# Performance work log

Measured on AMD Instinct MI355X. Metric: run time of the kernel, lower is better.

The kernel has to match this reference:

```python
import jax, jax.numpy as jnp
import numpy as np

N = 8192
IN_F = 512
OUT_F = 64
NEG_SLOPE = 0.01  # nn.LeakyReLU default
MASK_VAL = -1e9


def setup_inputs() -> dict:
    key = jax.random.key(0)
    k_h, k_adj, k_W, k_a = jax.random.split(key, 4)
    h = jax.random.normal(k_h, (N, IN_F), dtype=jnp.float32)
    adjacency = jax.random.randint(k_adj, (N, N), 0, 2, dtype=jnp.int32)
    # xavier_uniform bounds
    bW = float(np.sqrt(6.0 / (IN_F + OUT_F)))
    ba = float(np.sqrt(6.0 / (2 * OUT_F + 1)))
    W = jax.random.uniform(k_W, (IN_F, OUT_F), minval=-bW, maxval=bW, dtype=jnp.float32)
    a = jax.random.uniform(k_a, (2 * OUT_F, 1), minval=-ba, maxval=ba, dtype=jnp.float32)
    return {"h": h, "adjacency": adjacency, "W": W, "a": a}


def reference(h, adjacency, W, a):
    WH = h @ W                                  # [N, out_f]
    wh1 = WH @ a[:OUT_F, :]                     # [N, 1]
    wh2 = WH @ a[OUT_F:, :]                     # [N, 1]
    e = jax.nn.leaky_relu(wh1 + wh2.T, negative_slope=NEG_SLOPE)  # [N, N]
    attnt = jnp.where(adjacency > 0, e, jnp.float32(MASK_VAL))
    attnt = jax.nn.softmax(attnt, axis=1)       # row-wise softmax
    hfirst = attnt @ WH                         # [N, out_f]
    return jax.nn.elu(hfirst)
```

## Files before the change

### kernel.cpp

```cpp
#include <hip/hip_runtime.h>
#include <hip/hip_bf16.h>

#define N 8192
#define IN_F 512
#define OUT_F 64
#define S_SPLIT 16
#define JT (N / S_SPLIT)
#define NB (N / 8)
#define LDP 536
#define WHB 128
#define PACKB ((N / 32) * (N / 256) * 4)
#define LOG2E 1.44269504088896340736f

typedef __attribute__((ext_vector_type(8))) short short8;
typedef __attribute__((ext_vector_type(4))) float floatx4;
typedef __attribute__((ext_vector_type(4))) int intx4;

__device__ inline short f2bf(float x) {
    __hip_bfloat16 b = __float2bfloat16(x);
    return __builtin_bit_cast(short, b);
}

__device__ inline float fexp2(float x) {
#if __has_builtin(__builtin_amdgcn_exp2f)
    return __builtin_amdgcn_exp2f(x);
#else
    return exp2f(x);
#endif
}

__global__ void k_wt(const float* __restrict__ W, short* __restrict__ WT) {
    int idx = blockIdx.x * 256 + threadIdx.x;
    int k = idx >> 6, f = idx & 63;
    WT[f * IN_F + k] = f2bf(W[k * OUT_F + f]);
}

__global__ __launch_bounds__(256) void k_packwh(const int* __restrict__ adj,
                                                unsigned* __restrict__ mask,
                                                const float* __restrict__ h,
                                                const short* __restrict__ WT,
                                                const float* __restrict__ a,
                                                short* __restrict__ WHbT,
                                                float* __restrict__ wh1,
                                                float* __restrict__ wh2) {
    __shared__ float tileS[4][OUT_F][17];
    int tid = threadIdx.x;

    if (blockIdx.x >= WHB) {
        int bid = blockIdx.x - WHB;
        int wv = (bid * 256 + tid) >> 6;
        int lane = tid & 63;
        const int* p = adj + (size_t)wv * 512 + lane;
        unsigned long long m0 = __ballot(p[0]   > 0);
        unsigned long long m1 = __ballot(p[64]  > 0);
        unsigned long long m2 = __ballot(p[128] > 0);
        unsigned long long m3 = __ballot(p[192] > 0);
        unsigned long long m4 = __ballot(p[256] > 0);
        unsigned long long m5 = __ballot(p[320] > 0);
        unsigned long long m6 = __ballot(p[384] > 0);
        unsigned long long m7 = __ballot(p[448] > 0);
        if (lane < 16) {
            unsigned long long s0 = (lane & 2) ? m1 : m0;
            unsigned long long s1 = (lane & 2) ? m3 : m2;
            unsigned long long s2 = (lane & 2) ? m5 : m4;
            unsigned long long s3 = (lane & 2) ? m7 : m6;
            unsigned long long t0 = (lane & 4) ? s1 : s0;
            unsigned long long t1 = (lane & 4) ? s3 : s2;
            unsigned long long u  = (lane & 8) ? t1 : t0;
            unsigned dw = (lane & 1) ? (unsigned)(u >> 32) : (unsigned)u;
            mask[wv * 16 + lane] = dw;
        }
        return;
    }

    int w = tid >> 6, lane = tid & 63;
    int n = lane & 15, q = lane >> 4;
    int i0 = (blockIdx.x * 4 + w) * 16;
    float (*tile)[17] = tileS[w];
    const float* hp = h + (size_t)(i0 + n) * IN_F + q * 8;
    floatx4 acc[4] = {};
#pragma unroll
    for (int k0 = 0; k0 < IN_F; k0 += 32) {
        floatx4 h0 = *(const floatx4*)(hp + k0);
        floatx4 h1 = *(const floatx4*)(hp + k0 + 4);
        short8 af;
#pragma unroll
        for (int j = 0; j < 4; j++) { af[j] = f2bf(h0[j]); af[j + 4] = f2bf(h1[j]); }
#pragma unroll
        for (int b = 0; b < 4; b++) {
            short8 bf_ = *(const short8*)(WT + (b * 16 + n) * IN_F + k0 + q * 8);
            acc[b] = __builtin_amdgcn_mfma_f32_16x16x32_bf16(af, bf_, acc[b], 0, 0, 0);
        }
    }
#pragma unroll
    for (int b = 0; b < 4; b++)
#pragma unroll
        for (int r = 0; r < 4; r++)
            tile[b * 16 + n][q * 4 + r] = acc[b][r];
    float a1v[4], a2v[4];
#pragma unroll
    for (int b = 0; b < 4; b++) { a1v[b] = a[b * 16 + n]; a2v[b] = a[OUT_F + b * 16 + n]; }
#pragma unroll
    for (int r = 0; r < 4; r++) {
        float s1 = 0.f, s2 = 0.f;
#pragma unroll
        for (int b = 0; b < 4; b++) { s1 += acc[b][r] * a1v[b]; s2 += acc[b][r] * a2v[b]; }
#pragma unroll
        for (int m = 1; m <= 8; m <<= 1) {
            s1 += __shfl_xor(s1, m, 64);
            s2 += __shfl_xor(s2, m, 64);
        }
        if (n == 0) {
            wh1[i0 + q * 4 + r] = s1 * LOG2E;
            wh2[i0 + q * 4 + r] = s2 * LOG2E;
        }
    }
    __syncthreads();
    const float* tc = tile[lane & 63];
    short8 s0, s1v;
#pragma unroll
    for (int k = 0; k < 8; k++) { s0[k] = f2bf(tc[k]); s1v[k] = f2bf(tc[k + 8]); }
    *(short8*)(WHbT + (size_t)lane * N + i0) = s0;
    *(short8*)(WHbT + (size_t)lane * N + i0 + 8) = s1v;
}

__global__ __launch_bounds__(256, 2) void k_attn(const unsigned char* __restrict__ mask,
                                                 const short* __restrict__ WHbT,
                                                 const float* __restrict__ wh1,
                                                 const float* __restrict__ wh2,
                                                 float* __restrict__ num_part,
                                                 float* __restrict__ den_part) {
    __shared__ short ldsb[OUT_F * LDP];
    int tid = threadIdx.x;
    int w = tid >> 6;
    int lane = tid & 63;
    int n = lane & 15, q = lane >> 4;
    int split = blockIdx.y;
    int j0 = split * JT;
    int i0 = blockIdx.x * 256 + w * 64;

#pragma unroll
    for (int l = 0; l < 16; l++) {
        int idx = l * 256 + tid;
        int f = idx >> 6, c16 = idx & 63;
        short8 v = *(const short8*)(WHbT + (size_t)f * N + j0 + c16 * 8);
        *(short8*)(ldsb + f * LDP + c16 * 8) = v;
    }
    __syncthreads();

    float wh1f[4];
#pragma unroll
    for (int rf = 0; rf < 4; rf++) wh1f[rf] = wh1[i0 + rf * 16 + n];

    floatx4 acc[4][4] = {};
    floatx4 accd[4] = {};
    const float* w2p = wh2 + j0 + q * 8;
    const short* lp = ldsb + q * 8;
    int qs = q * 8;

    short8 onesf = {};
    if (n == 0) {
        short o = f2bf(1.0f);
#pragma unroll
        for (int jj = 0; jj < 8; jj++) onesf[jj] = o;
    }

    intx4 mcur[4], mnxt[4];
#pragma unroll
    for (int rf = 0; rf < 4; rf++)
        mcur[rf] = *(const intx4*)(mask + (size_t)(i0 + rf * 16 + n) * NB + split * 64);

    for (int g = 0; g < 4; g++) {
        if (g < 3) {
#pragma unroll
            for (int rf = 0; rf < 4; rf++)
                mnxt[rf] = *(const intx4*)(mask + (size_t)(i0 + rf * 16 + n) * NB
                                           + split * 64 + (g + 1) * 16);
        }
#pragma unroll
        for (int d = 0; d < 4; d++) {
            int s = g * 4 + d;
            floatx4 w20 = *(const floatx4*)(w2p + s * 32);
            floatx4 w21 = *(const floatx4*)(w2p + s * 32 + 4);
            short8 bfr[4];
#pragma unroll
            for (int b = 0; b < 4; b++)
                bfr[b] = *(const short8*)(lp + (b * 16 + n) * LDP + s * 32);
#pragma unroll
            for (int rf = 0; rf < 4; rf++) {
                unsigned md = (unsigned)mcur[rf][d] >> qs;
                float p[8];
#pragma unroll
                for (int jj = 0; jj < 8; jj++) {
                    float e = wh1f[rf] + ((jj < 4) ? w20[jj] : w21[jj - 4]);
                    float el = fmaxf(e, 0.01f * e);
                    el = ((md >> jj) & 1u) ? el : -1024.0f;
                    p[jj] = fexp2(el);
                }
                short8 af;
#pragma unroll
                for (int jj = 0; jj < 8; jj++) af[jj] = f2bf(p[jj]);
#pragma unroll
                for (int b = 0; b < 4; b++)
                    acc[rf][b] = __builtin_amdgcn_mfma_f32_16x16x32_bf16(af, bfr[b], acc[rf][b], 0, 0, 0);
                accd[rf] = __builtin_amdgcn_mfma_f32_16x16x32_bf16(af, onesf, accd[rf], 0, 0, 0);
            }
        }
#pragma unroll
        for (int rf = 0; rf < 4; rf++) mcur[rf] = mnxt[rf];
    }

#pragma unroll
    for (int rf = 0; rf < 4; rf++)
        if (n == 0)
            *(floatx4*)(den_part + (size_t)split * N + i0 + rf * 16 + q * 4) = accd[rf];

    float* np_ = num_part + (size_t)split * N * OUT_F;
#pragma unroll
    for (int rf = 0; rf < 4; rf++)
#pragma unroll
        for (int b = 0; b < 4; b++)
#pragma unroll
            for (int r = 0; r < 4; r++)
                np_[(size_t)(i0 + rf * 16 + q * 4 + r) * OUT_F + b * 16 + n] = acc[rf][b][r];
}

__global__ void k_final(const float* __restrict__ num_part,
                        const float* __restrict__ den_part,
                        float* __restrict__ out) {
    int idx = blockIdx.x * 256 + threadIdx.x;
    int row = idx >> 6;
    float s = 0.f, d = 0.f;
#pragma unroll
    for (int sp = 0; sp < S_SPLIT; sp++) {
        s += num_part[(size_t)sp * N * OUT_F + idx];
        d += den_part[sp * N + row];
    }
    float x = s / d;
    out[idx] = (x > 0.f) ? x : (__expf(x) - 1.f);
}

extern "C" void kernel_launch(void* const* d_in, const int* in_sizes, int n_in,
                              void* d_out, int out_size, void* d_ws, size_t ws_size,
                              hipStream_t stream) {
    const float* h = (const float*)d_in[0];
    const int* adj = (const int*)d_in[1];
    const float* W = (const float*)d_in[2];
    const float* a = (const float*)d_in[3];
    float* out = (float*)d_out;

    char* ws = (char*)d_ws;
    short* WHbT     = (short*)(ws);
    short* WT       = (short*)(ws + (size_t)(1 << 20));
    float* wh1      = (float*)(ws + (size_t)(1 << 20) + (64 << 10));
    float* wh2      = wh1 + N;
    unsigned* maskb = (unsigned*)(ws + (size_t)(2 << 20));
    float* num_p    = (float*)(ws + (size_t)(16 << 20));
    float* den_p    = (float*)(ws + (size_t)(48 << 20));

    k_wt<<<dim3(128), dim3(256), 0, stream>>>(W, WT);
    k_packwh<<<dim3(WHB + PACKB), dim3(256), 0, stream>>>(adj, maskb, h, WT, a,
                                                          WHbT, wh1, wh2);
    k_attn<<<dim3(N / 256, S_SPLIT), dim3(256), 0, stream>>>((const unsigned char*)maskb,
                                                             WHbT, wh1, wh2, num_p, den_p);
    k_final<<<dim3((N * OUT_F) / 256), dim3(256), 0, stream>>>(num_p, den_p, out);
}
```

Measured before the change: 398.2 us.

## Stream WH B-fragments from global with double-buffered registers instead of LDS; vectorize final reduce

The attention kernel no longer stages its 64x512 bf16 slice of WH^T in shared memory. Each wave loads its MFMA B fragments straight from global/L2 into two register buffers, prefetching step s+1 while computing step s. Mask words are now loaded at the top of each group instead of prefetched one group ahead, and launch bounds are raised to 3 blocks per CU. This removes the LDS fill, the barrier and the LDS occupancy limit, at the cost of redundant global loads across waves and more register pressure. The final reduction kernel now handles four outputs per thread with float4 loads and stores.

```diff
diff --git a/kernel.cpp b/kernel.cpp
--- a/kernel.cpp
+++ b/kernel.cpp
@@ -7,7 +7,6 @@
 #define S_SPLIT 16
 #define JT (N / S_SPLIT)
 #define NB (N / 8)
-#define LDP 536
 #define WHB 128
 #define PACKB ((N / 32) * (N / 256) * 4)
 #define LOG2E 1.44269504088896340736f
@@ -124,13 +123,12 @@
     *(short8*)(WHbT + (size_t)lane * N + i0 + 8) = s1v;
 }
 
-__global__ __launch_bounds__(256, 2) void k_attn(const unsigned char* __restrict__ mask,
+__global__ __launch_bounds__(256, 3) void k_attn(const unsigned char* __restrict__ mask,
                                                  const short* __restrict__ WHbT,
                                                  const float* __restrict__ wh1,
                                                  const float* __restrict__ wh2,
                                                  float* __restrict__ num_part,
                                                  float* __restrict__ den_part) {
-    __shared__ short ldsb[OUT_F * LDP];
     int tid = threadIdx.x;
     int w = tid >> 6;
     int lane = tid & 63;
@@ -139,14 +137,15 @@
     int j0 = split * JT;
     int i0 = blockIdx.x * 256 + w * 64;
 
-#pragma unroll
-    for (int l = 0; l < 16; l++) {
-        int idx = l * 256 + tid;
-        int f = idx >> 6, c16 = idx & 63;
-        short8 v = *(const short8*)(WHbT + (size_t)f * N + j0 + c16 * 8);
-        *(short8*)(ldsb + f * LDP + c16 * 8) = v;
-    }
-    __syncthreads();
+    const short* bbase = WHbT + j0 + q * 8;
+    short8 b0[4], b1[4];
+    auto bload = [&](short8* bb, int s) {
+        const short* bp = bbase + s * 32;
+#pragma unroll
+        for (int b = 0; b < 4; b++)
+            bb[b] = *(const short8*)(bp + (size_t)(b * 16 + n) * N);
+    };
+    bload(b0, 0);
 
     float wh1f[4];
 #pragma unroll
@@ -155,8 +154,6 @@
     floatx4 acc[4][4] = {};
     floatx4 accd[4] = {};
     const float* w2p = wh2 + j0 + q * 8;
-    const short* lp = ldsb + q * 8;
-    int qs = q * 8;
 
     short8 onesf = {};
     if (n == 0) {
@@ -165,30 +162,23 @@
         for (int jj = 0; jj < 8; jj++) onesf[jj] = o;
     }
 
-    intx4 mcur[4], mnxt[4];
-#pragma unroll
-    for (int rf = 0; rf < 4; rf++)
-        mcur[rf] = *(const intx4*)(mask + (size_t)(i0 + rf * 16 + n) * NB + split * 64);
-
+#pragma unroll
     for (int g = 0; g < 4; g++) {
-        if (g < 3) {
-#pragma unroll
-            for (int rf = 0; rf < 4; rf++)
-                mnxt[rf] = *(const intx4*)(mask + (size_t)(i0 + rf * 16 + n) * NB
-                                           + split * 64 + (g + 1) * 16);
-        }
+        intx4 mc[4];
+#pragma unroll
+        for (int rf = 0; rf < 4; rf++)
+            mc[rf] = *(const intx4*)(mask + (size_t)(i0 + rf * 16 + n) * NB
+                                     + split * 64 + g * 16);
 #pragma unroll
         for (int d = 0; d < 4; d++) {
             int s = g * 4 + d;
+            if (s < 15) bload((s & 1) ? b0 : b1, s + 1);
+            const short8* bb = (s & 1) ? b1 : b0;
             floatx4 w20 = *(const floatx4*)(w2p + s * 32);
             floatx4 w21 = *(const floatx4*)(w2p + s * 32 + 4);
-            short8 bfr[4];
-#pragma unroll
-            for (int b = 0; b < 4; b++)
-                bfr[b] = *(const short8*)(lp + (b * 16 + n) * LDP + s * 32);
 #pragma unroll
             for (int rf = 0; rf < 4; rf++) {
-                unsigned md = (unsigned)mcur[rf][d] >> qs;
+                unsigned md = (unsigned)mc[rf][d] >> (q * 8);
                 float p[8];
 #pragma unroll
                 for (int jj = 0; jj < 8; jj++) {
@@ -202,12 +192,10 @@
                 for (int jj = 0; jj < 8; jj++) af[jj] = f2bf(p[jj]);
 #pragma unroll
                 for (int b = 0; b < 4; b++)
-                    acc[rf][b] = __builtin_amdgcn_mfma_f32_16x16x32_bf16(af, bfr[b], acc[rf][b], 0, 0, 0);
+                    acc[rf][b] = __builtin_amdgcn_mfma_f32_16x16x32_bf16(af, bb[b], acc[rf][b], 0, 0, 0);
                 accd[rf] = __builtin_amdgcn_mfma_f32_16x16x32_bf16(af, onesf, accd[rf], 0, 0, 0);
             }
         }
-#pragma unroll
-        for (int rf = 0; rf < 4; rf++) mcur[rf] = mnxt[rf];
     }
 
 #pragma unroll
@@ -228,16 +216,24 @@
 __global__ void k_final(const float* __restrict__ num_part,
                         const float* __restrict__ den_part,
                         float* __restrict__ out) {
-    int idx = blockIdx.x * 256 + threadIdx.x;
-    int row = idx >> 6;
-    float s = 0.f, d = 0.f;
+    int t = blockIdx.x * 256 + threadIdx.x;
+    int idx4 = t * 4;
+    int row = idx4 >> 6;
+    floatx4 s = {};
+    float d = 0.f;
 #pragma unroll
     for (int sp = 0; sp < S_SPLIT; sp++) {
-        s += num_part[(size_t)sp * N * OUT_F + idx];
+        floatx4 v = *(const floatx4*)(num_part + (size_t)sp * N * OUT_F + idx4);
+        s += v;
         d += den_part[sp * N + row];
     }
-    float x = s / d;
-    out[idx] = (x > 0.f) ? x : (__expf(x) - 1.f);
+    floatx4 o;
+#pragma unroll
+    for (int j = 0; j < 4; j++) {
+        float x = s[j] / d;
+        o[j] = (x > 0.f) ? x : (__expf(x) - 1.f);
+    }
+    *(floatx4*)(out + idx4) = o;
 }
 
 extern "C" void kernel_launch(void* const* d_in, const int* in_sizes, int n_in,
@@ -263,5 +259,5 @@
                                                           WHbT, wh1, wh2);
     k_attn<<<dim3(N / 256, S_SPLIT), dim3(256), 0, stream>>>((const unsigned char*)maskb,
                                                              WHbT, wh1, wh2, num_p, den_p);
-    k_final<<<dim3((N * OUT_F) / 256), dim3(256), 0, stream>>>(num_p, den_p, out);
-}
+    k_final<<<dim3((N * OUT_F) / 1024), dim3(256), 0, stream>>>(num_p, den_p, out);
+}
```

Measured after the change: 420.2 us. 5.5% more time.

## Fuse split-K reduction into attention kernel via last-block atomic counter

Applied to the files above, without the earlier changes.

Removes the separate final reduction kernel. Each attention block increments a per-row-tile atomic counter after writing its partials, and the last of the 16 split blocks sums the partial numerators and denominators, then applies ELU and writes the output. Counters are zeroed in the weight-transpose kernel. This saves one kernel launch and lets the reduction overlap with other splits still running. In exchange it adds fences and atomics, and the reduction work for each row tile is serialized in a single tail block.

```diff
diff --git a/kernel.cpp b/kernel.cpp
--- a/kernel.cpp
+++ b/kernel.cpp
@@ -29,10 +29,12 @@
 #endif
 }
 
-__global__ void k_wt(const float* __restrict__ W, short* __restrict__ WT) {
+__global__ void k_wt(const float* __restrict__ W, short* __restrict__ WT,
+                     int* __restrict__ cnt) {
     int idx = blockIdx.x * 256 + threadIdx.x;
     int k = idx >> 6, f = idx & 63;
     WT[f * IN_F + k] = f2bf(W[k * OUT_F + f]);
+    if (blockIdx.x == 0 && threadIdx.x < 32) cnt[threadIdx.x] = 0;
 }
 
 __global__ __launch_bounds__(256) void k_packwh(const int* __restrict__ adj,
@@ -129,8 +131,11 @@
                                                  const float* __restrict__ wh1,
                                                  const float* __restrict__ wh2,
                                                  float* __restrict__ num_part,
-                                                 float* __restrict__ den_part) {
+                                                 float* __restrict__ den_part,
+                                                 int* __restrict__ cnt,
+                                                 float* __restrict__ out) {
     __shared__ short ldsb[OUT_F * LDP];
+    __shared__ int lastf;
     int tid = threadIdx.x;
     int w = tid >> 6;
     int lane = tid & 63;
@@ -223,21 +228,37 @@
 #pragma unroll
             for (int r = 0; r < 4; r++)
                 np_[(size_t)(i0 + rf * 16 + q * 4 + r) * OUT_F + b * 16 + n] = acc[rf][b][r];
-}
-
-__global__ void k_final(const float* __restrict__ num_part,
-                        const float* __restrict__ den_part,
-                        float* __restrict__ out) {
-    int idx = blockIdx.x * 256 + threadIdx.x;
-    int row = idx >> 6;
-    float s = 0.f, d = 0.f;
-#pragma unroll
-    for (int sp = 0; sp < S_SPLIT; sp++) {
-        s += num_part[(size_t)sp * N * OUT_F + idx];
-        d += den_part[sp * N + row];
-    }
-    float x = s / d;
-    out[idx] = (x > 0.f) ? x : (__expf(x) - 1.f);
+
+    __threadfence();
+    if (tid == 0) {
+        int old = __hip_atomic_fetch_add(&cnt[blockIdx.x], 1,
+                                         __ATOMIC_ACQ_REL, __HIP_MEMORY_SCOPE_AGENT);
+        lastf = (old == S_SPLIT - 1);
+    }
+    __syncthreads();
+    if (lastf) {
+        __threadfence();
+        size_t base = (size_t)blockIdx.x * 256 * OUT_F;
+#pragma unroll
+        for (int it = 0; it < 16; it++) {
+            size_t idx = base + (size_t)(it * 256 + tid) * 4;
+            int row = (int)(idx >> 6);
+            floatx4 s = {};
+            float dsum = 0.f;
+#pragma unroll
+            for (int sp = 0; sp < S_SPLIT; sp++) {
+                s += *(const floatx4*)(num_part + (size_t)sp * N * OUT_F + idx);
+                dsum += den_part[sp * N + row];
+            }
+            floatx4 o;
+#pragma unroll
+            for (int j = 0; j < 4; j++) {
+                float x = s[j] / dsum;
+                o[j] = (x > 0.f) ? x : (__expf(x) - 1.f);
+            }
+            *(floatx4*)(out + idx) = o;
+        }
+    }
 }
 
 extern "C" void kernel_launch(void* const* d_in, const int* in_sizes, int n_in,
@@ -257,11 +278,12 @@
     unsigned* maskb = (unsigned*)(ws + (size_t)(2 << 20));
     float* num_p    = (float*)(ws + (size_t)(16 << 20));
     float* den_p    = (float*)(ws + (size_t)(48 << 20));
-
-    k_wt<<<dim3(128), dim3(256), 0, stream>>>(W, WT);
+    int*   cnt      = (int*)(ws + (size_t)(49 << 20));
+
+    k_wt<<<dim3(128), dim3(256), 0, stream>>>(W, WT, cnt);
     k_packwh<<<dim3(WHB + PACKB), dim3(256), 0, stream>>>(adj, maskb, h, WT, a,
                                                           WHbT, wh1, wh2);
     k_attn<<<dim3(N / 256, S_SPLIT), dim3(256), 0, stream>>>((const unsigned char*)maskb,
-                                                             WHbT, wh1, wh2, num_p, den_p);
-    k_final<<<dim3((N * OUT_F) / 256), dim3(256), 0, stream>>>(num_p, den_p, out);
-}
+                                                             WHbT, wh1, wh2, num_p, den_p,
+                                                             cnt, out);
+}
```

Result: slower. 474.3 us (+19.1%).
